# Kernel tuning notes

Hardware: AMD Instinct MI355X
Metric: run time of the kernel (lower is better)

Reference implementation:

```python
import jax, jax.numpy as jnp
import numpy as np

DIM, NHEADS = 1024, 16
HD = DIM // NHEADS
ROPE_BASE = 10000.0


def rope_cos_sin(seq_len, hd):
    inv_freq = 1.0 / (ROPE_BASE ** (jnp.arange(0, hd, 2, dtype=jnp.float32) / hd))
    t = jnp.arange(seq_len, dtype=jnp.float32)
    freqs = jnp.outer(t, inv_freq)              # [N, hd/2]
    emb = jnp.concatenate([freqs, freqs], -1)   # [N, hd]
    return jnp.cos(emb), jnp.sin(emb)


def rotate_half(x):
    h = x.shape[-1] // 2
    return jnp.concatenate([-x[..., h:], x[..., :h]], -1)


def setup_inputs() -> dict:
    key = jax.random.key(0)
    ks = jax.random.split(key, 5)
    B, N = 1, 2048
    x = jax.random.normal(ks[0], (B, N, DIM), jnp.float32)
    wq = jax.random.normal(ks[1], (DIM, DIM), jnp.float32) * 0.02
    wk = jax.random.normal(ks[2], (DIM, DIM), jnp.float32) * 0.02
    wv = jax.random.normal(ks[3], (DIM, DIM), jnp.float32) * 0.02
    wp = jax.random.normal(ks[4], (DIM, DIM), jnp.float32) * 0.02
    return {"x": x, "wq": wq, "wk": wk, "wv": wv, "wp": wp}


def reference(x, wq, wk, wv, wp):
    B, N, D = x.shape
    H, hd = NHEADS, HD
    # nn.Linear: y = x @ W.T (weights stored [out, in])
    q = (x @ wq.T).reshape(B, N, H, hd)
    k = (x @ wk.T).reshape(B, N, H, hd)
    v = (x @ wv.T).reshape(B, N, H, hd)
    cos, sin = rope_cos_sin(N, hd)
    cos = cos[None, :, None, :]
    sin = sin[None, :, None, :]
    q = q * cos + rotate_half(q) * sin
    k = k * cos + rotate_half(k) * sin
    # SDPA (no mask, non-causal, eval -> no dropout)
    scale = 1.0 / jnp.sqrt(jnp.float32(hd))
    logits = jnp.einsum("bqhd,bkhd->bhqk", q, k) * scale
    attn = jax.nn.softmax(logits, axis=-1)
    out = jnp.einsum("bhqk,bkhd->bqhd", attn, v).reshape(B, N, D)
    return out @ wp.T
```

## Files before the change

kernel.cpp:

```cpp
#include <hip/hip_runtime.h>

typedef short s16x8 __attribute__((ext_vector_type(8)));
typedef float f32x4 __attribute__((ext_vector_type(4)));
typedef float f32x16 __attribute__((ext_vector_type(16)));
typedef unsigned int u32x4 __attribute__((ext_vector_type(4)));

__device__ __forceinline__ unsigned short f2bf(float f) {
    unsigned int u = __float_as_uint(f);
    u += 0x7fff + ((u >> 16) & 1);
    return (unsigned short)(u >> 16);
}
__device__ __forceinline__ float bf2f(unsigned short h) {
    return __uint_as_float(((unsigned int)h) << 16);
}
__device__ __forceinline__ unsigned pack2bf(float lo, float hi) {
    return (unsigned)f2bf(lo) | ((unsigned)f2bf(hi) << 16);
}
__device__ __forceinline__ f32x4 mfma16(s16x8 a, s16x8 b, f32x4 c) {
    return __builtin_amdgcn_mfma_f32_16x16x32_bf16(a, b, c, 0, 0, 0);
}
__device__ __forceinline__ f32x16 mfma32(s16x8 a, s16x8 b, f32x16 c) {
    return __builtin_amdgcn_mfma_f32_32x32x16_bf16(a, b, c, 0, 0, 0);
}
__device__ __forceinline__ void async16(const void* g, void* l) {
    __builtin_amdgcn_global_load_lds(
        (const __attribute__((address_space(1))) void*)g,
        (__attribute__((address_space(3))) void*)l, 16, 0, 0);
}

#define ROPE_C (-13.287712379549449f / 32.0f)

__global__ __launch_bounds__(256) void convert_all(
    const float* __restrict__ x,  const float* __restrict__ wq,
    const float* __restrict__ wk, const float* __restrict__ wv,
    const float* __restrict__ wp,
    unsigned short* __restrict__ xb, unsigned short* __restrict__ wqkvb,
    unsigned short* __restrict__ wpb)
{
    const size_t XN = 2048u * 1024u, WN = 1024u * 1024u;
    size_t e = ((size_t)blockIdx.x * 256 + threadIdx.x) * 4;
    const float* s; unsigned short* d;
    if (e < XN)                { s = x  + e;               d = xb    + e; }
    else if (e < XN + WN)      { s = wq + (e - XN);        d = wqkvb + (e - XN); }
    else if (e < XN + 2 * WN)  { s = wk + (e - XN - WN);   d = wqkvb + (e - XN); }
    else if (e < XN + 3 * WN)  { s = wv + (e - XN - 2*WN); d = wqkvb + (e - XN); }
    else                       { s = wp + (e - XN - 3*WN); d = wpb   + (e - XN - 3*WN); }
    float4 v = *(const float4*)s;
    ushort4 o;
    o.x = f2bf(v.x); o.y = f2bf(v.y); o.z = f2bf(v.z); o.w = f2bf(v.w);
    *(ushort4*)d = o;
}

template<int BM, int BN, int C32, int ROPE>
__global__ __launch_bounds__(256) void gemm_mfma(
    const unsigned short* __restrict__ A,
    const unsigned short* __restrict__ B,
    void* __restrict__ C, int Ntot)
{
    constexpr int MT = BM / 32, NT = BN / 32;
    __shared__ unsigned short As[BM * 64];
    __shared__ unsigned short Bs[BN * 64];

    const int tid  = threadIdx.x;
    const int wave = tid >> 6, lane = tid & 63;
    const int l16  = lane & 15, quad = lane >> 4;
    const int m0   = blockIdx.y * BM, n0 = blockIdx.x * BN;
    const int wm   = (wave & 1) * (BM / 2), wn = (wave >> 1) * (BN / 2);

    const int srow8 = lane >> 3;
    const int scol  = (lane & 7) * 8;

    f32x4 acc[MT][NT] = {};

    for (int k0 = 0; k0 < 1024; k0 += 64) {
        #pragma unroll
        for (int i = 0; i < BM / 32; i++) {
            int j = wave * (BM / 32) + i;
            async16(A + (size_t)(m0 + j * 8 + srow8) * 1024 + k0 + scol, &As[j * 512]);
        }
        #pragma unroll
        for (int i = 0; i < BN / 32; i++) {
            int j = wave * (BN / 32) + i;
            async16(B + (size_t)(n0 + j * 8 + srow8) * 1024 + k0 + scol, &Bs[j * 512]);
        }
        __syncthreads();

        #pragma unroll
        for (int ks = 0; ks < 2; ks++) {
            s16x8 af[MT], bfr[NT];
            #pragma unroll
            for (int mt = 0; mt < MT; mt++)
                af[mt] = *(const s16x8*)&As[(wm + mt * 16 + l16) * 64 + ks * 32 + quad * 8];
            #pragma unroll
            for (int nt = 0; nt < NT; nt++)
                bfr[nt] = *(const s16x8*)&Bs[(wn + nt * 16 + l16) * 64 + ks * 32 + quad * 8];
            #pragma unroll
            for (int mt = 0; mt < MT; mt++)
                #pragma unroll
                for (int nt = 0; nt < NT; nt++)
                    acc[mt][nt] = mfma16(af[mt], bfr[nt], acc[mt][nt]);
        }
        __syncthreads();
    }

    if constexpr (ROPE) {
        if (n0 < 2048) {
            #pragma unroll
            for (int mt = 0; mt < MT; mt++)
                #pragma unroll
                for (int r = 0; r < 4; r++) {
                    int m = m0 + wm + mt * 16 + quad * 4 + r;
                    #pragma unroll
                    for (int nt = 0; nt < 2; nt++) {
                        int i = nt * 16 + l16;
                        float ang = (float)m * exp2f((float)i * ROPE_C);
                        float c, s;
                        __sincosf(ang, &c, &s);
                        float e0 = acc[mt][nt][r], e1 = acc[mt][nt + 2][r];
                        acc[mt][nt][r]     = e0 * c + e1 * s;
                        acc[mt][nt + 2][r] = e1 * c - e0 * s;
                    }
                }
        }
    }

    #pragma unroll
    for (int mt = 0; mt < MT; mt++)
        #pragma unroll
        for (int nt = 0; nt < NT; nt++)
            #pragma unroll
            for (int r = 0; r < 4; r++) {
                int m = m0 + wm + mt * 16 + quad * 4 + r;
                int n = n0 + wn + nt * 16 + l16;
                size_t idx = (size_t)m * Ntot + n;
                if (C32) ((float*)C)[idx] = acc[mt][nt][r];
                else     ((unsigned short*)C)[idx] = f2bf(acc[mt][nt][r]);
            }
}

__global__ __launch_bounds__(256, 4) void attn_part(
    const unsigned short* __restrict__ qkv,
    unsigned short* __restrict__ Opart, float* __restrict__ Lpart)
{
    const int h  = blockIdx.y;
    const int q0 = blockIdx.x * 128;
    const int ks = blockIdx.z;
    const int tid  = threadIdx.x;
    const int wave = tid >> 6, lane = tid & 63;
    const int l32  = lane & 31, half = lane >> 5;

    __shared__ unsigned short Ks[64][72];
    __shared__ unsigned short Vt[64][72];

    const unsigned short* qp = qkv + (size_t)(q0 + wave * 32 + l32) * 3072 + h * 64 + half * 8;
    s16x8 qb[4];
    #pragma unroll
    for (int c = 0; c < 4; c++)
        qb[c] = *(const s16x8*)(qp + c * 16);

    f32x16 o0 = {}, o1 = {};
    float lsum = 0.f;

    for (int t = 0; t < 8; t++) {
        const int kt = ks * 512 + t * 64;

        if (tid < 128) {
            int g  = tid & 15;
            int d0 = (tid >> 4) * 8;
            const unsigned short* gv = qkv + (size_t)(kt + 4 * g) * 3072 + 2048 + h * 64 + d0;
            unsigned short a0[8], a1[8], a2[8], a3[8];
            *(uint4*)a0 = *(const uint4*)gv;
            *(uint4*)a1 = *(const uint4*)(gv + 3072);
            *(uint4*)a2 = *(const uint4*)(gv + 6144);
            *(uint4*)a3 = *(const uint4*)(gv + 9216);
            #pragma unroll
            for (int d = 0; d < 8; d++) {
                ushort4 w;
                w.x = a0[d]; w.y = a1[d]; w.z = a2[d]; w.w = a3[d];
                *(ushort4*)&Vt[d0 + d][4 * g] = w;
            }
        } else {
            int u = tid - 128;
            int key = u & 63;
            int dh = (u >> 6) * 32;
            const unsigned short* gk = qkv + (size_t)(kt + key) * 3072 + 1024 + h * 64 + dh;
            const uint4* g4 = (const uint4*)gk;
            uint4 k0 = g4[0], k1 = g4[1], k2 = g4[2], k3 = g4[3];
            *(uint4*)&Ks[key][dh]      = k0;
            *(uint4*)&Ks[key][dh + 8]  = k1;
            *(uint4*)&Ks[key][dh + 16] = k2;
            *(uint4*)&Ks[key][dh + 24] = k3;
        }
        __syncthreads();

        #pragma unroll
        for (int g = 0; g < 2; g++) {
            f32x16 s = {};
            #pragma unroll
            for (int c = 0; c < 4; c++) {
                s16x8 ka = *(const s16x8*)&Ks[g * 32 + l32][c * 16 + half * 8];
                s = mfma32(ka, qb[c], s);
            }
            #pragma unroll
            for (int f = 0; f < 2; f++) {
                float e[8];
                #pragma unroll
                for (int j = 0; j < 8; j++) {
                    e[j] = __expf(s[8 * f + j] * 0.125f);
                    lsum += e[j];
                }
                unsigned w0 = pack2bf(e[0], e[1]);
                unsigned w1 = pack2bf(e[2], e[3]);
                unsigned w2 = pack2bf(e[4], e[5]);
                unsigned w3 = pack2bf(e[6], e[7]);
                asm("v_permlane32_swap_b32 %0, %1" : "+v"(w0), "+v"(w2));
                asm("v_permlane32_swap_b32 %0, %1" : "+v"(w1), "+v"(w3));
                u32x4 wv; wv.x = w0; wv.y = w1; wv.z = w2; wv.w = w3;
                s16x8 pa = __builtin_bit_cast(s16x8, wv);
                const int c = 2 * g + f;
                s16x8 v0 = *(const s16x8*)&Vt[l32][c * 16 + half * 8];
                s16x8 v1 = *(const s16x8*)&Vt[32 + l32][c * 16 + half * 8];
                o0 = mfma32(pa, v0, o0);
                o1 = mfma32(pa, v1, o1);
            }
        }
        __syncthreads();
    }

    lsum += __shfl_xor(lsum, 32, 64);

    const int mq = q0 + wave * 32;
    unsigned short* opBase = Opart + (size_t)ks * 2048 * 1024;
    #pragma unroll
    for (int r = 0; r < 16; r++) {
        int qr = (r & 3) + 8 * (r >> 2) + 4 * half;
        unsigned short* op = opBase + (size_t)(mq + qr) * 1024 + h * 64;
        op[l32]      = f2bf(o0[r]);
        op[32 + l32] = f2bf(o1[r]);
    }
    if (half == 0)
        Lpart[((size_t)ks * 2048 + mq + l32) * 16 + h] = lsum;
}

__global__ __launch_bounds__(256) void combine(
    const unsigned short* __restrict__ Opart, const float* __restrict__ Lpart,
    unsigned short* __restrict__ ab)
{
    size_t e = ((size_t)blockIdx.x * 256 + threadIdx.x) * 4;
    int tok = (int)(e >> 10);
    int h = (int)((e & 1023) >> 6);
    float l = 0.f;
    #pragma unroll
    for (int s = 0; s < 4; s++)
        l += Lpart[((size_t)s * 2048 + tok) * 16 + h];
    float inv = 1.0f / l;
    float a0 = 0.f, a1 = 0.f, a2 = 0.f, a3 = 0.f;
    #pragma unroll
    for (int s = 0; s < 4; s++) {
        ushort4 n = *(const ushort4*)(Opart + (size_t)s * 2048 * 1024 + e);
        a0 += bf2f(n.x); a1 += bf2f(n.y); a2 += bf2f(n.z); a3 += bf2f(n.w);
    }
    ushort4 w;
    w.x = f2bf(a0 * inv);
    w.y = f2bf(a1 * inv);
    w.z = f2bf(a2 * inv);
    w.w = f2bf(a3 * inv);
    *(ushort4*)(ab + e) = w;
}

extern "C" void kernel_launch(void* const* d_in, const int* in_sizes, int n_in,
                              void* d_out, int out_size, void* d_ws, size_t ws_size,
                              hipStream_t stream)
{
    const float* x  = (const float*)d_in[0];
    const float* wq = (const float*)d_in[1];
    const float* wk = (const float*)d_in[2];
    const float* wv = (const float*)d_in[3];
    const float* wp = (const float*)d_in[4];

    unsigned short* xb    = (unsigned short*)d_ws;
    unsigned short* wqkvb = xb    + 2u * 1024 * 1024;
    unsigned short* wpb   = wqkvb + 3u * 1024 * 1024;
    unsigned short* qkv   = wpb   + 1u * 1024 * 1024;
    unsigned short* ab    = qkv   + 2048u * 3072;
    unsigned short* Opart = ab    + 2u * 1024 * 1024;
    float* Lpart = (float*)(Opart + 4u * 2048 * 1024);

    convert_all<<<6144, 256, 0, stream>>>(x, wq, wk, wv, wp, xb, wqkvb, wpb);
    gemm_mfma<64, 128, 0, 1><<<dim3(24, 32), 256, 0, stream>>>(
        xb, wqkvb, qkv, 3072);
    attn_part<<<dim3(16, 16, 4), 256, 0, stream>>>(qkv, Opart, Lpart);
    combine<<<2048, 256, 0, stream>>>(Opart, Lpart, ab);
    gemm_mfma<64, 64, 1, 0><<<dim3(16, 32), 256, 0, stream>>>(
        ab, wpb, d_out, 1024);
}
```

Measured before the change: 153.9 us.

## Double-buffer K/V tiles in attention and fold softmax scale into Q RoPE

The attention kernel now keeps two LDS buffers for K and transposed V. It issues the global loads for the next tile into registers before computing on the current tile, then writes them to the other buffer, so there is one barrier per iteration instead of two. The 1/sqrt(hd) scale moves into the Q projection's RoPE epilogue, which removes a multiply per logit from the exp loop. This doubles LDS use and adds register pressure for the prefetched data, which may reduce occupancy at 4 blocks per CU.

Result: slower. 242.0 us (+57.2%).

```diff
diff --git a/kernel.cpp b/kernel.cpp
--- a/kernel.cpp
+++ b/kernel.cpp
@@ -105,6 +105,7 @@
 
     if constexpr (ROPE) {
         if (n0 < 2048) {
+            const float sc = (n0 < 1024) ? 0.125f : 1.0f;
             #pragma unroll
             for (int mt = 0; mt < MT; mt++)
                 #pragma unroll
@@ -116,6 +117,7 @@
                         float ang = (float)m * exp2f((float)i * ROPE_C);
                         float c, s;
                         __sincosf(ang, &c, &s);
+                        c *= sc; s *= sc;
                         float e0 = acc[mt][nt][r], e1 = acc[mt][nt + 2][r];
                         acc[mt][nt][r]     = e0 * c + e1 * s;
                         acc[mt][nt + 2][r] = e1 * c - e0 * s;
@@ -149,8 +151,8 @@
     const int wave = tid >> 6, lane = tid & 63;
     const int l32  = lane & 31, half = lane >> 5;
 
-    __shared__ unsigned short Ks[64][72];
-    __shared__ unsigned short Vt[64][72];
+    __shared__ unsigned short Ks[2][64][72];
+    __shared__ unsigned short Vt[2][64][72];
 
     const unsigned short* qp = qkv + (size_t)(q0 + wave * 32 + l32) * 3072 + h * 64 + half * 8;
     s16x8 qb[4];
@@ -161,44 +163,65 @@
     f32x16 o0 = {}, o1 = {};
     float lsum = 0.f;
 
-    for (int t = 0; t < 8; t++) {
+    uint4 r0, r1, r2, r3;
+
+    auto issue = [&](int t) {
         const int kt = ks * 512 + t * 64;
-
         if (tid < 128) {
             int g  = tid & 15;
             int d0 = (tid >> 4) * 8;
             const unsigned short* gv = qkv + (size_t)(kt + 4 * g) * 3072 + 2048 + h * 64 + d0;
-            unsigned short a0[8], a1[8], a2[8], a3[8];
-            *(uint4*)a0 = *(const uint4*)gv;
-            *(uint4*)a1 = *(const uint4*)(gv + 3072);
-            *(uint4*)a2 = *(const uint4*)(gv + 6144);
-            *(uint4*)a3 = *(const uint4*)(gv + 9216);
-            #pragma unroll
-            for (int d = 0; d < 8; d++) {
-                ushort4 w;
-                w.x = a0[d]; w.y = a1[d]; w.z = a2[d]; w.w = a3[d];
-                *(ushort4*)&Vt[d0 + d][4 * g] = w;
-            }
+            r0 = *(const uint4*)gv;
+            r1 = *(const uint4*)(gv + 3072);
+            r2 = *(const uint4*)(gv + 6144);
+            r3 = *(const uint4*)(gv + 9216);
         } else {
             int u = tid - 128;
             int key = u & 63;
             int dh = (u >> 6) * 32;
             const unsigned short* gk = qkv + (size_t)(kt + key) * 3072 + 1024 + h * 64 + dh;
             const uint4* g4 = (const uint4*)gk;
-            uint4 k0 = g4[0], k1 = g4[1], k2 = g4[2], k3 = g4[3];
-            *(uint4*)&Ks[key][dh]      = k0;
-            *(uint4*)&Ks[key][dh + 8]  = k1;
-            *(uint4*)&Ks[key][dh + 16] = k2;
-            *(uint4*)&Ks[key][dh + 24] = k3;
-        }
-        __syncthreads();
+            r0 = g4[0]; r1 = g4[1]; r2 = g4[2]; r3 = g4[3];
+        }
+    };
+    auto commit = [&](int p) {
+        if (tid < 128) {
+            int g  = tid & 15;
+            int d0 = (tid >> 4) * 8;
+            unsigned short a0[8], a1[8], a2[8], a3[8];
+            *(uint4*)a0 = r0; *(uint4*)a1 = r1;
+            *(uint4*)a2 = r2; *(uint4*)a3 = r3;
+            #pragma unroll
+            for (int d = 0; d < 8; d++) {
+                ushort4 w;
+                w.x = a0[d]; w.y = a1[d]; w.z = a2[d]; w.w = a3[d];
+                *(ushort4*)&Vt[p][d0 + d][4 * g] = w;
+            }
+        } else {
+            int u = tid - 128;
+            int key = u & 63;
+            int dh = (u >> 6) * 32;
+            *(uint4*)&Ks[p][key][dh]      = r0;
+            *(uint4*)&Ks[p][key][dh + 8]  = r1;
+            *(uint4*)&Ks[p][key][dh + 16] = r2;
+            *(uint4*)&Ks[p][key][dh + 24] = r3;
+        }
+    };
+
+    issue(0);
+    commit(0);
+    __syncthreads();
+
+    for (int t = 0; t < 8; t++) {
+        const int p = t & 1;
+        if (t < 7) issue(t + 1);
 
         #pragma unroll
         for (int g = 0; g < 2; g++) {
             f32x16 s = {};
             #pragma unroll
             for (int c = 0; c < 4; c++) {
-                s16x8 ka = *(const s16x8*)&Ks[g * 32 + l32][c * 16 + half * 8];
+                s16x8 ka = *(const s16x8*)&Ks[p][g * 32 + l32][c * 16 + half * 8];
                 s = mfma32(ka, qb[c], s);
             }
             #pragma unroll
@@ -206,7 +229,7 @@
                 float e[8];
                 #pragma unroll
                 for (int j = 0; j < 8; j++) {
-                    e[j] = __expf(s[8 * f + j] * 0.125f);
+                    e[j] = __expf(s[8 * f + j]);
                     lsum += e[j];
                 }
                 unsigned w0 = pack2bf(e[0], e[1]);
@@ -218,12 +241,14 @@
                 u32x4 wv; wv.x = w0; wv.y = w1; wv.z = w2; wv.w = w3;
                 s16x8 pa = __builtin_bit_cast(s16x8, wv);
                 const int c = 2 * g + f;
-                s16x8 v0 = *(const s16x8*)&Vt[l32][c * 16 + half * 8];
-                s16x8 v1 = *(const s16x8*)&Vt[32 + l32][c * 16 + half * 8];
+                s16x8 v0 = *(const s16x8*)&Vt[p][l32][c * 16 + half * 8];
+                s16x8 v1 = *(const s16x8*)&Vt[p][32 + l32][c * 16 + half * 8];
                 o0 = mfma32(pa, v0, o0);
                 o1 = mfma32(pa, v1, o1);
             }
         }
+
+        if (t < 7) commit(p ^ 1);
         __syncthreads();
     }
 
```
